# Kernel optimization log

Measured on AMD Instinct MI355X. Metric: run time of the kernel, lower is better.

Reference implementation:

```python
import jax, jax.numpy as jnp
import numpy as np

B, T, C, H = 8, 1024, 1024, 16
D = C // H
EPS = 1e-5


def setup_inputs() -> dict:
    key = jax.random.key(0)
    ks = jax.random.split(key, 12)
    s = lambda k, shape, scale=0.02: jax.random.normal(k, shape, dtype=jnp.float32) * scale
    return {
        "x": jax.random.normal(ks[0], (B, T, C), dtype=jnp.float32),
        "ln1_w": jnp.ones((C,), jnp.float32),
        "ln1_b": jnp.zeros((C,), jnp.float32),
        "w_qkv": s(ks[1], (C, 3 * C)),
        "b_qkv": jnp.zeros((3 * C,), jnp.float32),
        "w_o": s(ks[2], (C, C)),
        "b_o": jnp.zeros((C,), jnp.float32),
        "ln2_w": jnp.ones((C,), jnp.float32),
        "ln2_b": jnp.zeros((C,), jnp.float32),
        "w_fc": s(ks[3], (C, 4 * C)),
        "b_fc": jnp.zeros((4 * C,), jnp.float32),
        "w_proj": s(ks[4], (4 * C, C)),
        "b_proj": jnp.zeros((C,), jnp.float32),
    }


def _layernorm(x, w, b):
    mu = jnp.mean(x, axis=-1, keepdims=True)
    var = jnp.mean(jnp.square(x - mu), axis=-1, keepdims=True)
    return (x - mu) * jax.lax.rsqrt(var + EPS) * w + b


def _attention(x, w_qkv, b_qkv, w_o, b_o):
    b, t, c = x.shape
    qkv = x @ w_qkv + b_qkv                      # [B,T,3C]
    q, k, v = jnp.split(qkv, 3, axis=-1)
    q = q.reshape(b, t, H, D)
    k = k.reshape(b, t, H, D)
    v = v.reshape(b, t, H, D)
    scores = jnp.einsum("bqhd,bkhd->bhqk", q, k) / jnp.sqrt(jnp.float32(D))
    mask = jnp.tril(jnp.ones((t, t), dtype=bool))  # causal
    scores = jnp.where(mask, scores, jnp.float32(-jnp.inf))
    att = jax.nn.softmax(scores, axis=-1)
    y = jnp.einsum("bhqk,bkhd->bqhd", att, v).reshape(b, t, c)
    return y @ w_o + b_o


def _mlp(x, w_fc, b_fc, w_proj, b_proj):
    h = jax.nn.gelu(x @ w_fc + b_fc, approximate=True)  # tanh GELU
    return h @ w_proj + b_proj


def reference(x, ln1_w, ln1_b, w_qkv, b_qkv, w_o, b_o, ln2_w, ln2_b, w_fc, b_fc, w_proj, b_proj):
    x = x + _attention(_layernorm(x, ln1_w, ln1_b), w_qkv, b_qkv, w_o, b_o)
    x = x + _mlp(_layernorm(x, ln2_w, ln2_b), w_fc, b_fc, w_proj, b_proj)
    return x
```

## Files before the change

### kernel.cpp

```cpp
#include <hip/hip_runtime.h>
#include <math.h>
#include <stdint.h>

typedef unsigned short u16;
typedef unsigned int u32;
typedef __attribute__((ext_vector_type(4))) unsigned short u16x4;
typedef __attribute__((ext_vector_type(8))) unsigned short u16x8;
typedef __attribute__((ext_vector_type(8))) __bf16 bf16x8;
typedef __attribute__((ext_vector_type(4))) float f32x4;

#define Bn 8
#define Tn 1024
#define Cn 1024
#define Hn 16
#define Dn 64
#define Mn 8192

#define F32_ONE_BITS 0x3F800000u

__device__ __forceinline__ float b2f(u16 u) {
  union { unsigned int i; float f; } v; v.i = ((unsigned int)u) << 16; return v.f;
}
__device__ __forceinline__ u16 f2b(float f) {
  union { float f; unsigned int i; } v; v.f = f;
  unsigned int r = v.i + 0x7fffu + ((v.i >> 16) & 1u);
  return (u16)(r >> 16);
}

__device__ __forceinline__ void async_ld16(const u16* g, u16* l) {
  __builtin_amdgcn_global_load_lds(
      (__attribute__((address_space(1))) void*)g,
      (__attribute__((address_space(3))) void*)l, 16, 0, 0);
}

__device__ __forceinline__ float gelu_tanh(float x) {
  float x3 = x * x * x;
  float t = tanhf(0.7978845608028654f * (x + 0.044715f * x3));
  return 0.5f * x * (1.0f + t);
}

__global__ __launch_bounds__(256) void cvt_x_k(const void* __restrict__ src, u16* __restrict__ dst,
                                               const u32* __restrict__ flagp) {
  bool isf32 = (*flagp == F32_ONE_BITS);
  size_t i = ((size_t)blockIdx.x * 256 + threadIdx.x) * 4;
  if (isf32) {
    f32x4 v = *reinterpret_cast<const f32x4*>((const float*)src + i);
    u16x4 o;
#pragma unroll
    for (int j = 0; j < 4; j++) o[j] = f2b(v[j]);
    *reinterpret_cast<u16x4*>(dst + i) = o;
  } else {
    *reinterpret_cast<u16x4*>(dst + i) = *reinterpret_cast<const u16x4*>((const u16*)src + i);
  }
}

struct SmallCvt { const void* src[8]; u16* dst[8]; int n[8]; };

__global__ __launch_bounds__(256) void cvt_small_k(SmallCvt p, const u32* __restrict__ flagp) {
  bool isf32 = (*flagp == F32_ONE_BITS);
  int t = blockIdx.x * 256 + threadIdx.x;
  int off = 0;
#pragma unroll
  for (int i = 0; i < 8; i++) {
    int idx = t - off;
    if (idx >= 0 && idx < p.n[i]) {
      u16 v = isf32 ? f2b(((const float*)p.src[i])[idx]) : ((const u16*)p.src[i])[idx];
      p.dst[i][idx] = v;
    }
    off += p.n[i];
  }
}

__global__ __launch_bounds__(256) void transpose_k(const void* __restrict__ in,
                                                   u16* __restrict__ out, int K, int N,
                                                   const u32* __restrict__ flagp) {
  bool isf32 = (*flagp == F32_ONE_BITS);
  __shared__ u16 tile[32][33];
  int c0 = blockIdx.x * 32, r0 = blockIdx.y * 32;
  int tx = threadIdx.x, ty = threadIdx.y;
#pragma unroll
  for (int i = 0; i < 4; i++) {
    size_t idx = (size_t)(r0 + ty + i * 8) * N + c0 + tx;
    tile[ty + i * 8][tx] = isf32 ? f2b(((const float*)in)[idx]) : ((const u16*)in)[idx];
  }
  __syncthreads();
#pragma unroll
  for (int i = 0; i < 4; i++)
    out[(size_t)(c0 + ty + i * 8) * K + r0 + tx] = tile[tx][ty + i * 8];
}

__global__ __launch_bounds__(256) void ln_k(const u16* __restrict__ x, const u16* __restrict__ w,
                                            const u16* __restrict__ bi, u16* __restrict__ out) {
  int row = blockIdx.x, tid = threadIdx.x;
  const u16* xr = x + (size_t)row * Cn;
  u16x4 xv = *reinterpret_cast<const u16x4*>(xr + tid * 4);
  float v0 = b2f(xv[0]), v1 = b2f(xv[1]), v2 = b2f(xv[2]), v3 = b2f(xv[3]);
  float s = v0 + v1 + v2 + v3;
  float s2 = v0 * v0 + v1 * v1 + v2 * v2 + v3 * v3;
#pragma unroll
  for (int m = 1; m < 64; m <<= 1) {
    s += __shfl_xor(s, m, 64);
    s2 += __shfl_xor(s2, m, 64);
  }
  __shared__ float rs_[4], rs2_[4];
  int wave = tid >> 6, lane = tid & 63;
  if (lane == 0) { rs_[wave] = s; rs2_[wave] = s2; }
  __syncthreads();
  s = rs_[0] + rs_[1] + rs_[2] + rs_[3];
  s2 = rs2_[0] + rs2_[1] + rs2_[2] + rs2_[3];
  float mu = s * (1.0f / Cn);
  float var = s2 * (1.0f / Cn) - mu * mu;
  float rstd = rsqrtf(var + 1e-5f);
  u16x4 wv = *reinterpret_cast<const u16x4*>(w + tid * 4);
  u16x4 bv = *reinterpret_cast<const u16x4*>(bi + tid * 4);
  u16x4 ov;
  float vv[4] = {v0, v1, v2, v3};
#pragma unroll
  for (int j = 0; j < 4; j++)
    ov[j] = f2b((vv[j] - mu) * rstd * b2f(wv[j]) + b2f(bv[j]));
  *reinterpret_cast<u16x4*>(out + (size_t)row * Cn + tid * 4) = ov;
}

template <int GELU, int RES, int F32OUT>
__global__ __launch_bounds__(256) void gemm_k(const u16* __restrict__ A, const u16* __restrict__ BT,
                                              const u16* __restrict__ bias, const u16* __restrict__ res,
                                              void* __restrict__ Cout, int M, int N, int K) {
  __shared__ __align__(16) u16 As[128 * 32];
  __shared__ __align__(16) u16 Bs[128 * 32];
  int tid = threadIdx.x, wave = tid >> 6, lane = tid & 63;
  int l15 = lane & 15, quad = lane >> 4;
  int m0 = blockIdx.y * 128, n0 = blockIdx.x * 128;
  int wm = (wave & 1) * 64, wn = (wave >> 1) * 64;

  int offA[4], offB[4];
#pragma unroll
  for (int i = 0; i < 4; i++) {
    int rowA = wm + i * 16 + l15;
    offA[i] = rowA * 32 + ((quad ^ (rowA >> 1)) & 3) * 8;
    int rowB = wn + i * 16 + l15;
    offB[i] = rowB * 32 + ((quad ^ (rowB >> 1)) & 3) * 8;
  }

  const u16 *aSrc[2], *bSrc[2];
  u16 *aDst[2], *bDst[2];
#pragma unroll
  for (int i = 0; i < 2; i++) {
    int c = wave * 128 + i * 64 + lane;
    int row = c >> 2;
    int kc = ((c & 3) ^ ((row >> 1) & 3));
    aSrc[i] = A + (size_t)(m0 + row) * K + kc * 8;
    bSrc[i] = BT + (size_t)(n0 + row) * K + kc * 8;
    aDst[i] = As + (size_t)(wave * 128 + i * 64) * 8;
    bDst[i] = Bs + (size_t)(wave * 128 + i * 64) * 8;
  }

  f32x4 acc[4][4];
#pragma unroll
  for (int mi = 0; mi < 4; mi++)
#pragma unroll
    for (int ni = 0; ni < 4; ni++) acc[mi][ni] = (f32x4){0.f, 0.f, 0.f, 0.f};

  for (int k0 = 0; k0 < K; k0 += 32) {
    __syncthreads();
    async_ld16(aSrc[0] + k0, aDst[0]);
    async_ld16(aSrc[1] + k0, aDst[1]);
    async_ld16(bSrc[0] + k0, bDst[0]);
    async_ld16(bSrc[1] + k0, bDst[1]);
    __syncthreads();
    bf16x8 av[4], bv[4];
#pragma unroll
    for (int i = 0; i < 4; i++) av[i] = *reinterpret_cast<const bf16x8*>(As + offA[i]);
#pragma unroll
    for (int i = 0; i < 4; i++) bv[i] = *reinterpret_cast<const bf16x8*>(Bs + offB[i]);
#pragma unroll
    for (int mi = 0; mi < 4; mi++)
#pragma unroll
      for (int ni = 0; ni < 4; ni++)
        acc[mi][ni] = __builtin_amdgcn_mfma_f32_16x16x32_bf16(av[mi], bv[ni], acc[mi][ni], 0, 0, 0);
  }

#pragma unroll
  for (int ni = 0; ni < 4; ni++) {
    int col = n0 + wn + ni * 16 + l15;
    float bval = b2f(bias[col]);
#pragma unroll
    for (int mi = 0; mi < 4; mi++) {
#pragma unroll
      for (int r = 0; r < 4; r++) {
        int row = m0 + wm + mi * 16 + quad * 4 + r;
        float v = acc[mi][ni][r] + bval;
        if (GELU) v = gelu_tanh(v);
        if (RES) v += b2f(res[(size_t)row * N + col]);
        if (F32OUT)
          ((float*)Cout)[(size_t)row * N + col] = v;
        else
          ((u16*)Cout)[(size_t)row * N + col] = f2b(v);
      }
    }
  }
}

__global__ __launch_bounds__(256) void attn_k(const u16* __restrict__ qkv, u16* __restrict__ y) {
  int qt = blockIdx.x, bh = blockIdx.y;
  int b = bh >> 4, h = bh & 15;
  int tid = threadIdx.x, wave = tid >> 6, lane = tid & 63;
  int l15 = lane & 15, quad = lane >> 4;

  __shared__ __align__(16) u16 Ks[64 * 72];
  __shared__ __align__(16) u16 VTs[64 * 72];
  __shared__ __align__(16) u16 Ps[4][16 * 72];

  const u16* base = qkv + (size_t)b * Tn * 3072 + h * 64;
  int q0 = qt * 64 + wave * 16;

  bf16x8 qfrag[2];
#pragma unroll
  for (int kc = 0; kc < 2; kc++)
    qfrag[kc] = *reinterpret_cast<const bf16x8*>(base + (size_t)(q0 + l15) * 3072 + kc * 32 + quad * 8);

  f32x4 o[4];
#pragma unroll
  for (int dn = 0; dn < 4; dn++) o[dn] = (f32x4){0.f, 0.f, 0.f, 0.f};
  float m_r[4] = {-1e30f, -1e30f, -1e30f, -1e30f};
  float l_r[4] = {0.f, 0.f, 0.f, 0.f};

  int kvend = qt * 64;
  for (int kv0 = 0; kv0 <= kvend; kv0 += 64) {
    __syncthreads();
    {
      int key = tid >> 2, d0 = (tid & 3) * 16;
      const u16* kp = base + 1024 + (size_t)(kv0 + key) * 3072 + d0;
      u16x8 ka = *reinterpret_cast<const u16x8*>(kp);
      u16x8 kb = *reinterpret_cast<const u16x8*>(kp + 8);
      *reinterpret_cast<u16x8*>(&Ks[key * 72 + d0]) = ka;
      *reinterpret_cast<u16x8*>(&Ks[key * 72 + d0 + 8]) = kb;
      const u16* vp = base + 2048 + (size_t)(kv0 + key) * 3072 + d0;
      u16x8 va = *reinterpret_cast<const u16x8*>(vp);
      u16x8 vb = *reinterpret_cast<const u16x8*>(vp + 8);
#pragma unroll
      for (int i = 0; i < 8; i++) {
        VTs[(d0 + i) * 72 + key] = va[i];
        VTs[(d0 + 8 + i) * 72 + key] = vb[i];
      }
    }
    __syncthreads();

    float sv[4][4];
#pragma unroll
    for (int ni = 0; ni < 4; ni++) {
      f32x4 z = (f32x4){0.f, 0.f, 0.f, 0.f};
#pragma unroll
      for (int kc = 0; kc < 2; kc++) {
        bf16x8 bfr = *reinterpret_cast<const bf16x8*>(&Ks[(ni * 16 + l15) * 72 + kc * 32 + quad * 8]);
        z = __builtin_amdgcn_mfma_f32_16x16x32_bf16(qfrag[kc], bfr, z, 0, 0, 0);
      }
#pragma unroll
      for (int r = 0; r < 4; r++) sv[ni][r] = z[r];
    }
    bool diag = (kv0 + 64 > q0);
#pragma unroll
    for (int ni = 0; ni < 4; ni++)
#pragma unroll
      for (int r = 0; r < 4; r++) {
        float v = sv[ni][r] * 0.125f;
        if (diag && (kv0 + ni * 16 + l15 > q0 + quad * 4 + r)) v = -1e30f;
        sv[ni][r] = v;
      }
    float mt[4], al[4], rs[4];
#pragma unroll
    for (int r = 0; r < 4; r++) {
      mt[r] = fmaxf(fmaxf(sv[0][r], sv[1][r]), fmaxf(sv[2][r], sv[3][r]));
#pragma unroll
      for (int m = 1; m <= 8; m <<= 1) mt[r] = fmaxf(mt[r], __shfl_xor(mt[r], m, 64));
      float mn = fmaxf(m_r[r], mt[r]);
      al[r] = __expf(m_r[r] - mn);
      m_r[r] = mn;
      rs[r] = 0.f;
    }
#pragma unroll
    for (int ni = 0; ni < 4; ni++)
#pragma unroll
      for (int r = 0; r < 4; r++) {
        float p = __expf(sv[ni][r] - m_r[r]);
        sv[ni][r] = p;
        rs[r] += p;
      }
#pragma unroll
    for (int r = 0; r < 4; r++) {
#pragma unroll
      for (int m = 1; m <= 8; m <<= 1) rs[r] += __shfl_xor(rs[r], m, 64);
      l_r[r] = l_r[r] * al[r] + rs[r];
    }
#pragma unroll
    for (int dn = 0; dn < 4; dn++)
#pragma unroll
      for (int r = 0; r < 4; r++) o[dn][r] *= al[r];
#pragma unroll
    for (int ni = 0; ni < 4; ni++)
#pragma unroll
      for (int r = 0; r < 4; r++)
        Ps[wave][(quad * 4 + r) * 72 + ni * 16 + l15] = f2b(sv[ni][r]);
#pragma unroll
    for (int kc = 0; kc < 2; kc++) {
      bf16x8 afr = *reinterpret_cast<const bf16x8*>(&Ps[wave][l15 * 72 + kc * 32 + quad * 8]);
#pragma unroll
      for (int dn = 0; dn < 4; dn++) {
        bf16x8 bfr = *reinterpret_cast<const bf16x8*>(&VTs[(dn * 16 + l15) * 72 + kc * 32 + quad * 8]);
        o[dn] = __builtin_amdgcn_mfma_f32_16x16x32_bf16(afr, bfr, o[dn], 0, 0, 0);
      }
    }
  }
#pragma unroll
  for (int r = 0; r < 4; r++) {
    float inv = 1.0f / l_r[r];
    int row = b * Tn + q0 + quad * 4 + r;
#pragma unroll
    for (int dn = 0; dn < 4; dn++)
      y[(size_t)row * Cn + h * 64 + dn * 16 + l15] = f2b(o[dn][r] * inv);
  }
}

extern "C" void kernel_launch(void* const* d_in, const int* in_sizes, int n_in,
                              void* d_out, int out_size, void* d_ws, size_t ws_size,
                              hipStream_t stream) {
  const void* x      = d_in[0];
  const void* ln1_w  = d_in[1];
  const void* ln1_b  = d_in[2];
  const void* w_qkv  = d_in[3];
  const void* b_qkv  = d_in[4];
  const void* w_o    = d_in[5];
  const void* b_o    = d_in[6];
  const void* ln2_w  = d_in[7];
  const void* ln2_b  = d_in[8];
  const void* w_fc   = d_in[9];
  const void* b_fc   = d_in[10];
  const void* w_proj = d_in[11];
  const void* b_proj = d_in[12];
  const u32* flagp = (const u32*)ln1_w;

  size_t off = 0;
  char* wsb = (char*)d_ws;
  auto alloc = [&](size_t bytes) {
    void* p = wsb + off;
    off += (bytes + 255) & ~(size_t)255;
    return (u16*)p;
  };
  u16* wqkvT  = alloc((size_t)3072 * 1024 * 2);
  u16* woT    = alloc((size_t)1024 * 1024 * 2);
  u16* wfcT   = alloc((size_t)4096 * 1024 * 2);
  u16* wprojT = alloc((size_t)1024 * 4096 * 2);
  u16* xb     = alloc((size_t)Mn * 1024 * 2);
  u16* sm     = alloc((size_t)16384 * 2);
  u16* xn     = alloc((size_t)Mn * 1024 * 2);
  u16* ybuf   = alloc((size_t)Mn * 1024 * 2);
  u16* x1     = alloc((size_t)Mn * 1024 * 2);
  u16* big    = alloc((size_t)Mn * 4096 * 2);
  u16* qkvbuf = big;
  u16* hbuf   = big;
  if (off > ws_size) return;

  u16* LW1 = sm;
  u16* LB1 = sm + 1024;
  u16* BQKV = sm + 2048;
  u16* BO  = sm + 5120;
  u16* LW2 = sm + 6144;
  u16* LB2 = sm + 7168;
  u16* BFC = sm + 8192;
  u16* BPJ = sm + 12288;

  SmallCvt sc;
  sc.src[0] = ln1_w;  sc.dst[0] = LW1;  sc.n[0] = 1024;
  sc.src[1] = ln1_b;  sc.dst[1] = LB1;  sc.n[1] = 1024;
  sc.src[2] = b_qkv;  sc.dst[2] = BQKV; sc.n[2] = 3072;
  sc.src[3] = b_o;    sc.dst[3] = BO;   sc.n[3] = 1024;
  sc.src[4] = ln2_w;  sc.dst[4] = LW2;  sc.n[4] = 1024;
  sc.src[5] = ln2_b;  sc.dst[5] = LB2;  sc.n[5] = 1024;
  sc.src[6] = b_fc;   sc.dst[6] = BFC;  sc.n[6] = 4096;
  sc.src[7] = b_proj; sc.dst[7] = BPJ;  sc.n[7] = 1024;

  hipLaunchKernelGGL(cvt_small_k, dim3(52), dim3(256), 0, stream, sc, flagp);
  hipLaunchKernelGGL(cvt_x_k, dim3(Mn * 1024 / 4 / 256), dim3(256), 0, stream, x, xb, flagp);

  dim3 tb(32, 8);
  hipLaunchKernelGGL(transpose_k, dim3(3072 / 32, 1024 / 32), tb, 0, stream, w_qkv, wqkvT, 1024, 3072, flagp);
  hipLaunchKernelGGL(transpose_k, dim3(1024 / 32, 1024 / 32), tb, 0, stream, w_o, woT, 1024, 1024, flagp);
  hipLaunchKernelGGL(transpose_k, dim3(4096 / 32, 1024 / 32), tb, 0, stream, w_fc, wfcT, 1024, 4096, flagp);
  hipLaunchKernelGGL(transpose_k, dim3(1024 / 32, 4096 / 32), tb, 0, stream, w_proj, wprojT, 4096, 1024, flagp);

  hipLaunchKernelGGL(ln_k, dim3(Mn), dim3(256), 0, stream, xb, LW1, LB1, xn);
  hipLaunchKernelGGL((gemm_k<0, 0, 0>), dim3(3072 / 128, Mn / 128), dim3(256), 0, stream,
                     xn, wqkvT, BQKV, (const u16*)nullptr, (void*)qkvbuf, Mn, 3072, 1024);
  hipLaunchKernelGGL(attn_k, dim3(Tn / 64, Bn * Hn), dim3(256), 0, stream, qkvbuf, ybuf);
  hipLaunchKernelGGL((gemm_k<0, 1, 0>), dim3(1024 / 128, Mn / 128), dim3(256), 0, stream,
                     ybuf, woT, BO, xb, (void*)x1, Mn, 1024, 1024);
  hipLaunchKernelGGL(ln_k, dim3(Mn), dim3(256), 0, stream, x1, LW2, LB2, xn);
  hipLaunchKernelGGL((gemm_k<1, 0, 0>), dim3(4096 / 128, Mn / 128), dim3(256), 0, stream,
                     xn, wfcT, BFC, (const u16*)nullptr, (void*)hbuf, Mn, 4096, 1024);
  hipLaunchKernelGGL((gemm_k<0, 1, 1>), dim3(1024 / 128, Mn / 128), dim3(256), 0, stream,
                     hbuf, wprojT, BPJ, x1, d_out, Mn, 1024, 4096);
}
```

Before: 625.5 us.

## Pre-transpose V in global memory and read attention K/V fragments directly

Adds a separate kernel that transposes the V slice of the QKV buffer into a per-head [D, T] layout. The attention kernel now drops its shared-memory staging of K and V and loads the MFMA operand fragments straight from global memory. The aim is to remove the scalar, bank-conflicting LDS transpose of V and the two block-wide barriers per KV tile. In exchange it adds an extra kernel launch plus a write and read of V. The four waves now fetch the same K and V data separately, relying on cache, and the global-load latency is exposed with no prefetching.

```diff
diff --git a/kernel.cpp b/kernel.cpp
--- a/kernel.cpp
+++ b/kernel.cpp
@@ -87,6 +87,22 @@
 #pragma unroll
   for (int i = 0; i < 4; i++)
     out[(size_t)(c0 + ty + i * 8) * K + r0 + tx] = tile[tx][ty + i * 8];
+}
+
+__global__ __launch_bounds__(256) void attn_vt_k(const u16* __restrict__ qkv, u16* __restrict__ vT) {
+  __shared__ u16 tile[32][33];
+  int t0 = blockIdx.x * 32;
+  int bh = blockIdx.y >> 1, dt = blockIdx.y & 1;
+  int b = bh >> 4, h = bh & 15;
+  int d0 = dt * 32;
+  int tx = threadIdx.x, ty = threadIdx.y;
+#pragma unroll
+  for (int i = 0; i < 4; i++)
+    tile[ty + i * 8][tx] = qkv[(size_t)(b * Tn + t0 + ty + i * 8) * 3072 + 2048 + h * 64 + d0 + tx];
+  __syncthreads();
+#pragma unroll
+  for (int i = 0; i < 4; i++)
+    vT[((size_t)bh * 64 + d0 + ty + i * 8) * Tn + t0 + tx] = tile[tx][ty + i * 8];
 }
 
 __global__ __launch_bounds__(256) void ln_k(const u16* __restrict__ x, const u16* __restrict__ w,
@@ -200,17 +216,18 @@
   }
 }
 
-__global__ __launch_bounds__(256) void attn_k(const u16* __restrict__ qkv, u16* __restrict__ y) {
+__global__ __launch_bounds__(256) void attn_k(const u16* __restrict__ qkv, const u16* __restrict__ vT,
+                                              u16* __restrict__ y) {
   int qt = blockIdx.x, bh = blockIdx.y;
   int b = bh >> 4, h = bh & 15;
   int tid = threadIdx.x, wave = tid >> 6, lane = tid & 63;
   int l15 = lane & 15, quad = lane >> 4;
 
-  __shared__ __align__(16) u16 Ks[64 * 72];
-  __shared__ __align__(16) u16 VTs[64 * 72];
   __shared__ __align__(16) u16 Ps[4][16 * 72];
 
   const u16* base = qkv + (size_t)b * Tn * 3072 + h * 64;
+  const u16* kbase = base + 1024;
+  const u16* vbase = vT + (size_t)bh * 64 * Tn;
   int q0 = qt * 64 + wave * 16;
 
   bf16x8 qfrag[2];
@@ -226,33 +243,15 @@
 
   int kvend = qt * 64;
   for (int kv0 = 0; kv0 <= kvend; kv0 += 64) {
-    __syncthreads();
-    {
-      int key = tid >> 2, d0 = (tid & 3) * 16;
-      const u16* kp = base + 1024 + (size_t)(kv0 + key) * 3072 + d0;
-      u16x8 ka = *reinterpret_cast<const u16x8*>(kp);
-      u16x8 kb = *reinterpret_cast<const u16x8*>(kp + 8);
-      *reinterpret_cast<u16x8*>(&Ks[key * 72 + d0]) = ka;
-      *reinterpret_cast<u16x8*>(&Ks[key * 72 + d0 + 8]) = kb;
-      const u16* vp = base + 2048 + (size_t)(kv0 + key) * 3072 + d0;
-      u16x8 va = *reinterpret_cast<const u16x8*>(vp);
-      u16x8 vb = *reinterpret_cast<const u16x8*>(vp + 8);
-#pragma unroll
-      for (int i = 0; i < 8; i++) {
-        VTs[(d0 + i) * 72 + key] = va[i];
-        VTs[(d0 + 8 + i) * 72 + key] = vb[i];
-      }
-    }
-    __syncthreads();
-
     float sv[4][4];
 #pragma unroll
     for (int ni = 0; ni < 4; ni++) {
       f32x4 z = (f32x4){0.f, 0.f, 0.f, 0.f};
 #pragma unroll
       for (int kc = 0; kc < 2; kc++) {
-        bf16x8 bfr = *reinterpret_cast<const bf16x8*>(&Ks[(ni * 16 + l15) * 72 + kc * 32 + quad * 8]);
-        z = __builtin_amdgcn_mfma_f32_16x16x32_bf16(qfrag[kc], bfr, z, 0, 0, 0);
+        bf16x8 kfr = *reinterpret_cast<const bf16x8*>(
+            kbase + (size_t)(kv0 + ni * 16 + l15) * 3072 + kc * 32 + quad * 8);
+        z = __builtin_amdgcn_mfma_f32_16x16x32_bf16(qfrag[kc], kfr, z, 0, 0, 0);
       }
 #pragma unroll
       for (int r = 0; r < 4; r++) sv[ni][r] = z[r];
@@ -300,12 +299,14 @@
 #pragma unroll
       for (int r = 0; r < 4; r++)
         Ps[wave][(quad * 4 + r) * 72 + ni * 16 + l15] = f2b(sv[ni][r]);
+    __syncthreads();
 #pragma unroll
     for (int kc = 0; kc < 2; kc++) {
       bf16x8 afr = *reinterpret_cast<const bf16x8*>(&Ps[wave][l15 * 72 + kc * 32 + quad * 8]);
 #pragma unroll
       for (int dn = 0; dn < 4; dn++) {
-        bf16x8 bfr = *reinterpret_cast<const bf16x8*>(&VTs[(dn * 16 + l15) * 72 + kc * 32 + quad * 8]);
+        bf16x8 bfr = *reinterpret_cast<const bf16x8*>(
+            vbase + (size_t)(dn * 16 + l15) * Tn + kv0 + kc * 32 + quad * 8);
         o[dn] = __builtin_amdgcn_mfma_f32_16x16x32_bf16(afr, bfr, o[dn], 0, 0, 0);
       }
     }
@@ -357,6 +358,7 @@
   u16* big    = alloc((size_t)Mn * 4096 * 2);
   u16* qkvbuf = big;
   u16* hbuf   = big;
+  u16* vTbuf  = big + (size_t)Mn * 3072;
   if (off > ws_size) return;
 
   u16* LW1 = sm;
@@ -390,7 +392,8 @@
   hipLaunchKernelGGL(ln_k, dim3(Mn), dim3(256), 0, stream, xb, LW1, LB1, xn);
   hipLaunchKernelGGL((gemm_k<0, 0, 0>), dim3(3072 / 128, Mn / 128), dim3(256), 0, stream,
                      xn, wqkvT, BQKV, (const u16*)nullptr, (void*)qkvbuf, Mn, 3072, 1024);
-  hipLaunchKernelGGL(attn_k, dim3(Tn / 64, Bn * Hn), dim3(256), 0, stream, qkvbuf, ybuf);
+  hipLaunchKernelGGL(attn_vt_k, dim3(Tn / 32, Bn * Hn * 2), tb, 0, stream, qkvbuf, vTbuf);
+  hipLaunchKernelGGL(attn_k, dim3(Tn / 64, Bn * Hn), dim3(256), 0, stream, qkvbuf, vTbuf, ybuf);
   hipLaunchKernelGGL((gemm_k<0, 1, 0>), dim3(1024 / 128, Mn / 128), dim3(256), 0, stream,
                      ybuf, woT, BO, xb, (void*)x1, Mn, 1024, 1024);
   hipLaunchKernelGGL(ln_k, dim3(Mn), dim3(256), 0, stream, x1, LW2, LB2, xn);
```

Result: slower. 752.0 us (+20.2%).
